# Optimization experiments

Measured on AMD Instinct MI355X. Metric: run time of the kernel, lower is better.

The kernel has to match this reference:

```python
import jax, jax.numpy as jnp
from jax import lax
import numpy as np

B, T, I, H, O = 2048, 512, 3, 128, 2


def _uniform(key, shape, scale):
    return jax.random.uniform(key, shape, jnp.float32, -scale, scale)


def setup_inputs() -> dict:
    key = jax.random.key(0)
    ks = jax.random.split(key, 12)
    s = 1.0 / np.sqrt(H)  # PyTorch LSTM init scale
    inp = {
        "x": jax.random.normal(ks[0], (B, T, I), jnp.float32),
        # layer 0: input size I
        "w_ih0": _uniform(ks[1], (4 * H, I), s),
        "w_hh0": _uniform(ks[2], (4 * H, H), s),
        "b_ih0": _uniform(ks[3], (4 * H,), s),
        "b_hh0": _uniform(ks[4], (4 * H,), s),
        # layer 1: input size H
        "w_ih1": _uniform(ks[5], (4 * H, H), s),
        "w_hh1": _uniform(ks[6], (4 * H, H), s),
        "b_ih1": _uniform(ks[7], (4 * H,), s),
        "b_hh1": _uniform(ks[8], (4 * H,), s),
        # final projection
        "fc_w": _uniform(ks[9], (O, H), 1.0 / np.sqrt(H)),
        "fc_b": _uniform(ks[10], (O,), 1.0 / np.sqrt(H)),
    }
    return inp


def _lstm_layer(x, w_ih, w_hh, b_ih, b_hh):
    # x: [B, T, D_in] -> hidden sequence [B, T, H]
    b, t, _ = x.shape
    h_dim = w_hh.shape[1]
    # precompute input projections for all timesteps (one big GEMM)
    x_proj = jnp.einsum("btd,gd->btg", x, w_ih) + b_ih + b_hh  # [B, T, 4H]
    x_proj = jnp.swapaxes(x_proj, 0, 1)  # [T, B, 4H]

    def step(carry, xt):
        h, c = carry
        gates = xt + h @ w_hh.T  # [B, 4H]
        i, f, g, o = jnp.split(gates, 4, axis=-1)  # PyTorch gate order i,f,g,o
        i = jax.nn.sigmoid(i)
        f = jax.nn.sigmoid(f)
        g = jnp.tanh(g)
        o = jax.nn.sigmoid(o)
        c = f * c + i * g
        h = o * jnp.tanh(c)
        return (h, c), h

    h0 = jnp.zeros((b, h_dim), x.dtype)
    c0 = jnp.zeros((b, h_dim), x.dtype)
    _, hs = lax.scan(step, (h0, c0), x_proj)  # hs: [T, B, H]
    return jnp.swapaxes(hs, 0, 1)  # [B, T, H]


def reference(x, w_ih0, w_hh0, b_ih0, b_hh0, w_ih1, w_hh1, b_ih1, b_hh1, fc_w, fc_b):
    h1 = _lstm_layer(x, w_ih0, w_hh0, b_ih0, b_hh0)   # [B, T, H]
    h2 = _lstm_layer(h1, w_ih1, w_hh1, b_ih1, b_hh1)  # [B, T, H]
    last = h2[:, -1, :]                                # [B, H]
    return last @ fc_w.T + fc_b                        # [B, O]
```

## Files before the change

### kernel.cpp

```cpp
#include <hip/hip_runtime.h>

#define B_   2048
#define T_   512
#define H_   128
#define G_   512
#define R_   8
#define NTHR 512

typedef _Float16 f16;
typedef _Float16 f16x8 __attribute__((ext_vector_type(8)));
typedef float    f32x4 __attribute__((ext_vector_type(4)));
typedef int      i32x2 __attribute__((ext_vector_type(2)));

#define OFF_W1    0
#define OFF_RING  131072
#define OFF_HB    139264
#define OFF_XT    143360
#define LDS_BYTES 145408

__device__ __forceinline__ float rcp_(float v) {
#if __has_builtin(__builtin_amdgcn_rcpf)
  return __builtin_amdgcn_rcpf(v);
#else
  return 1.0f / v;
#endif
}
__device__ __forceinline__ float sig_(float v)  { return rcp_(1.0f + __expf(-v)); }
__device__ __forceinline__ float tanh_(float v) { return 1.0f - 2.0f * rcp_(__expf(2.0f * v) + 1.0f); }

__device__ __forceinline__ f16x8 cvt8(const float* __restrict__ p) {
  float4 a = ((const float4*)p)[0];
  float4 b = ((const float4*)p)[1];
  f16x8 v;
  v[0]=(f16)a.x; v[1]=(f16)a.y; v[2]=(f16)a.z; v[3]=(f16)a.w;
  v[4]=(f16)b.x; v[5]=(f16)b.y; v[6]=(f16)b.z; v[7]=(f16)b.w;
  return v;
}
__device__ __forceinline__ f32x4 mfma16(f16x8 a, f16x8 b, f32x4 c) {
  return __builtin_amdgcn_mfma_f32_16x16x32_f16(a, b, c, 0, 0, 0);
}

__device__ __forceinline__ void pls2_(float a, float b, float& x, float& y) {
#if __has_builtin(__builtin_amdgcn_permlane32_swap)
  i32x2 r = __builtin_amdgcn_permlane32_swap(__float_as_int(a), __float_as_int(b),
                                             false, false);
  x = __int_as_float(r.x); y = __int_as_float(r.y);
#else
  asm volatile("v_permlane32_swap_b32 %0, %1" : "+v"(a), "+v"(b));
  x = a; y = b;
#endif
}

__global__ __launch_bounds__(NTHR, 2)
void lstm_v11(const float* __restrict__ x,
              const float* __restrict__ w_ih0, const float* __restrict__ w_hh0,
              const float* __restrict__ b_ih0, const float* __restrict__ b_hh0,
              const float* __restrict__ w_ih1, const float* __restrict__ w_hh1,
              const float* __restrict__ b_ih1, const float* __restrict__ b_hh1,
              const float* __restrict__ fc_w,  const float* __restrict__ fc_b,
              float* __restrict__ out)
{
  extern __shared__ char lds[];
  char*  w1L   = lds + OFF_W1;
  char*  ringB = lds + OFF_RING;
  char*  hBB   = lds + OFF_HB;
  char*  xT    = lds + OFF_XT;

  const int tid  = (int)threadIdx.x;
  const int lane = tid & 63;
  const int wv   = tid >> 6;
  const int n    = lane & 15;
  const int hi   = lane >> 4;
  const int u0   = wv * 16;
  const int blk  = (int)blockIdx.x;
  const int rsw  = (n & 7) << 4;

  for (int idx = tid; idx < 8192; idx += NTHR) {
    const int g  = idx >> 4, c  = idx & 15;
    const int w  = (g >> 4) & 7, nn = g & 15, q = g >> 7;
    const int kc = c >> 2,  hh = c & 3;
    f16x8 v = cvt8(w_ih1 + g*H_ + c*8);
    *(f16x8*)(w1L + w*16384 + (q*4+kc)*1024 + ((hh<<4) + nn)*16) = v;
  }
  for (int i = tid; i < 3584; i += NTHR) ((unsigned*)ringB)[i] = 0u;
  __syncthreads();

  float xr0 = 0.f, xr1 = 0.f, xr2 = 0.f;
  if (wv == 7) {
    const int tok = lane >> 3, r = lane & 7;
    const size_t base = (size_t)(blk*R_ + r) * T_;
    const float a0 = x[(base + tok)*3+0];
    const float a1 = x[(base + tok)*3+1];
    const float a2 = x[(base + tok)*3+2];
    f16* w = (f16*)(xT + tok*128 + r*16);
    w[0] = (f16)a0; w[1] = (f16)a1; w[2] = (f16)a2;
    xr0 = x[(base + 8 + tok)*3+0];
    xr1 = x[(base + 8 + tok)*3+1];
    xr2 = x[(base + 8 + tok)*3+2];
  }

  f16x8 whh0f[4][4], whh1f[4][4];
  #pragma unroll
  for (int q = 0; q < 4; ++q)
    #pragma unroll
    for (int kc = 0; kc < 4; ++kc) {
      const int off = (q*H_ + u0 + n)*H_ + kc*32 + hi*8;
      whh0f[q][kc] = cvt8(w_hh0 + off);
      whh1f[q][kc] = cvt8(w_hh1 + off);
    }
  f16x8 w0p[4];
  float b0[4], bP[4];
  #pragma unroll
  for (int q = 0; q < 4; ++q) {
    const int g = q*H_ + u0 + n;
    b0[q] = b_ih0[g] + b_hh0[g];
    bP[q] = b_ih1[g] + b_hh1[g];
    f16x8 z;
    #pragma unroll
    for (int e = 0; e < 8; ++e) z[e] = (f16)0.f;
    if (hi == 0) {
      z[0] = (f16)w_ih0[g*3+0];
      z[1] = (f16)w_ih0[g*3+1];
      z[2] = (f16)w_ih0[g*3+2];
    }
    w0p[q] = z;
  }

  int offA[4];
  #pragma unroll
  for (int kc = 0; kc < 4; ++kc)
    offA[kc] = (n&7)*256 + ((kc*64 + hi*16) ^ rsw);

  float cA0 = 0.f, cA1 = 0.f, cB0 = 0.f, cB1 = 0.f;
  f32x4 xpP[4];
  const int rowbase = (hi & 1)*4 + ((lane >= 32) ? 2 : 0);
  const int colb    = 2*(u0 + n);
  const int wOff0 = rowbase*256     + (colb ^ (rowbase<<4));
  const int wOff1 = (rowbase+1)*256 + (colb ^ ((rowbase+1)<<4));
  const char* __restrict__ w1lane = w1L + wv*16384 + lane*16;
  __syncthreads();

  auto xstage = [&](int s) {
    if (wv == 7 && (s & 7) == 3) {
      const int c = s >> 3;
      const int tok = lane >> 3, r = lane & 7;
      if (c <= 61) {
        const size_t base = (size_t)(blk*R_ + r) * T_ + (8*(c+2) + tok);
        const float a0 = x[base*3+0], a1 = x[base*3+1], a2 = x[base*3+2];
        f16* w = (f16*)(xT + ((c+1)&1)*1024 + tok*128 + r*16);
        w[0] = (f16)xr0; w[1] = (f16)xr1; w[2] = (f16)xr2;
        xr0 = a0; xr1 = a1; xr2 = a2;
      } else if (c == 62) {
        f16* w = (f16*)(xT + ((c+1)&1)*1024 + tok*128 + r*16);
        w[0] = (f16)xr0; w[1] = (f16)xr1; w[2] = (f16)xr2;
      }
    }
  };

  auto proj = [&](int s) {
    if ((s & 1) == 0 && s >= 2 && s <= T_) {
      const char* pa = ringB + ((n < 8) ? (((s-2)&3)*2048) : (((s-1)&3)*2048));
      #pragma unroll
      for (int q = 0; q < 4; ++q)
        { xpP[q][0]=bP[q]; xpP[q][1]=bP[q]; xpP[q][2]=bP[q]; xpP[q][3]=bP[q]; }
      #pragma unroll
      for (int kc = 0; kc < 4; ++kc) {
        const f16x8 a = *(const f16x8*)(pa + offA[kc]);
        #pragma unroll
        for (int q = 0; q < 4; ++q) {
          const f16x8 bf = *(const f16x8*)(w1lane + (q*4 + kc)*1024);
          xpP[q] = mfma16(a, bf, xpP[q]);
        }
      }
    }
  };

  auto l0 = [&](int s) {
    if (s < T_) {
      const f16x8 ax = *(const f16x8*)(xT + ((s>>3)&1)*1024 + (s&7)*128 + (n&7)*16);
      f32x4 acc[4];
      #pragma unroll
      for (int q = 0; q < 4; ++q) {
        f32x4 a; a[0]=b0[q]; a[1]=b0[q]; a[2]=b0[q]; a[3]=b0[q];
        acc[q] = mfma16(ax, w0p[q], a);
      }
      const char* pa = ringB + (((s-1)&3)*2048);
      #pragma unroll
      for (int kc = 0; kc < 4; ++kc) {
        const f16x8 af = *(const f16x8*)(pa + offA[kc]);
        #pragma unroll
        for (int q = 0; q < 4; ++q) acc[q] = mfma16(af, whh0f[q][kc], acc[q]);
      }
      char* wr = ringB + ((s&3)*2048);
      float gA[4], gB[4], d0, d1;
      #pragma unroll
      for (int q = 0; q < 4; ++q) {
        pls2_(acc[q][0], acc[q][2], gA[q], d0);
        pls2_(acc[q][1], acc[q][3], gB[q], d1);
      }
      {
        const float iv = sig_(gA[0]), fv = sig_(gA[1]), gv = tanh_(gA[2]), ov = sig_(gA[3]);
        cA0 = fv*cA0 + iv*gv;
        *(f16*)(wr + wOff0) = (f16)(ov * tanh_(cA0));
      }
      {
        const float iv = sig_(gB[0]), fv = sig_(gB[1]), gv = tanh_(gB[2]), ov = sig_(gB[3]);
        cA1 = fv*cA1 + iv*gv;
        *(f16*)(wr + wOff1) = (f16)(ov * tanh_(cA1));
      }
    }
  };

  auto l1 = [&](int s) {
    if (s >= 2) {
      const bool odd = (s & 1);
      const char* pb = hBB + (s&1)*2048;
      f32x4 acc[4];
      #pragma unroll
      for (int q = 0; q < 4; ++q) acc[q] = xpP[q];
      #pragma unroll
      for (int kc = 0; kc < 4; ++kc) {
        const f16x8 af = *(const f16x8*)(pb + offA[kc]);
        #pragma unroll
        for (int q = 0; q < 4; ++q) acc[q] = mfma16(af, whh1f[q][kc], acc[q]);
      }
      char* wr = hBB + (((s+1)&1)*2048);
      float gA[4], gB[4];
      #pragma unroll
      for (int q = 0; q < 4; ++q) {
        float ex, ey, fx, fy;
        pls2_(acc[q][0], acc[q][2], ex, ey);
        pls2_(acc[q][1], acc[q][3], fx, fy);
        gA[q] = odd ? ey : ex;
        gB[q] = odd ? fy : fx;
      }
      {
        const float iv = sig_(gA[0]), fv = sig_(gA[1]), gv = tanh_(gA[2]), ov = sig_(gA[3]);
        cB0 = fv*cB0 + iv*gv;
        *(f16*)(wr + wOff0) = (f16)(ov * tanh_(cB0));
      }
      {
        const float iv = sig_(gB[0]), fv = sig_(gB[1]), gv = tanh_(gB[2]), ov = sig_(gB[3]);
        cB1 = fv*cB1 + iv*gv;
        *(f16*)(wr + wOff1) = (f16)(ov * tanh_(cB1));
      }
    }
  };

  for (int s = 0; s < T_ + 2; ++s) {
    if (wv & 1) {
      xstage(s);
      l0(s);
      proj(s);
      l1(s);
    } else {
      proj(s);
      l1(s);
      l0(s);
    }
    __syncthreads();
  }

  if (tid < R_*2) {
    const int r = tid >> 1, o = tid & 1;
    float acc = fc_b[o];
    #pragma unroll 4
    for (int d = 0; d < H_; ++d) {
      const f16 hv = *(const f16*)(hBB + r*256 + ((2*d) ^ ((r&7)<<4)));
      acc += (float)hv * fc_w[o*H_ + d];
    }
    out[(blk*R_ + r)*2 + o] = acc;
  }
}

extern "C" void kernel_launch(void* const* d_in, const int* in_sizes, int n_in,
                              void* d_out, int out_size, void* d_ws, size_t ws_size,
                              hipStream_t stream) {
  const float* x     = (const float*)d_in[0];
  const float* w_ih0 = (const float*)d_in[1];
  const float* w_hh0 = (const float*)d_in[2];
  const float* b_ih0 = (const float*)d_in[3];
  const float* b_hh0 = (const float*)d_in[4];
  const float* w_ih1 = (const float*)d_in[5];
  const float* w_hh1 = (const float*)d_in[6];
  const float* b_ih1 = (const float*)d_in[7];
  const float* b_hh1 = (const float*)d_in[8];
  const float* fc_w  = (const float*)d_in[9];
  const float* fc_b  = (const float*)d_in[10];
  (void)in_sizes; (void)n_in; (void)out_size; (void)d_ws; (void)ws_size;

  hipFuncSetAttribute((const void*)lstm_v11,
                      hipFuncAttributeMaxDynamicSharedMemorySize, LDS_BYTES);

  lstm_v11<<<B_/R_, NTHR, LDS_BYTES, stream>>>(
      x, w_ih0, w_hh0, b_ih0, b_hh0, w_ih1, w_hh1, b_ih1, b_hh1,
      fc_w, fc_b, (float*)d_out);
}
```

Before: 857.2 us.

## Split layer-0 and layer-1 LSTM work across separate wave groups

The block grows to 1024 threads. Waves 0-7 run the layer-0 recurrence and waves 8-15 run the layer-1 input projection and recurrence, where before every wave interleaved both layers. The layer-0 input projection now uses a K=16 MFMA with the bias folded in as a constant-one input column, and the xT staging buffer doubles in size. The aim is to shorten each wave's serial per-step chain and halve per-wave register pressure. In exchange, each SIMD hosts more waves and every step synchronises 16 waves at the barrier.

```diff
diff --git a/kernel.cpp b/kernel.cpp
--- a/kernel.cpp
+++ b/kernel.cpp
@@ -5,9 +5,10 @@
 #define H_   128
 #define G_   512
 #define R_   8
-#define NTHR 512
+#define NTHR 1024
 
 typedef _Float16 f16;
+typedef _Float16 f16x4 __attribute__((ext_vector_type(4)));
 typedef _Float16 f16x8 __attribute__((ext_vector_type(8)));
 typedef float    f32x4 __attribute__((ext_vector_type(4)));
 typedef int      i32x2 __attribute__((ext_vector_type(2)));
@@ -16,7 +17,7 @@
 #define OFF_RING  131072
 #define OFF_HB    139264
 #define OFF_XT    143360
-#define LDS_BYTES 145408
+#define LDS_BYTES 147456
 
 __device__ __forceinline__ float rcp_(float v) {
 #if __has_builtin(__builtin_amdgcn_rcpf)
@@ -38,6 +39,9 @@
 }
 __device__ __forceinline__ f32x4 mfma16(f16x8 a, f16x8 b, f32x4 c) {
   return __builtin_amdgcn_mfma_f32_16x16x32_f16(a, b, c, 0, 0, 0);
+}
+__device__ __forceinline__ f32x4 mfma16k16(f16x4 a, f16x4 b, f32x4 c) {
+  return __builtin_amdgcn_mfma_f32_16x16x16f16(a, b, c, 0, 0, 0);
 }
 
 __device__ __forceinline__ void pls2_(float a, float b, float& x, float& y) {
@@ -51,8 +55,8 @@
 #endif
 }
 
-__global__ __launch_bounds__(NTHR, 2)
-void lstm_v11(const float* __restrict__ x,
+__global__ __launch_bounds__(NTHR)
+void lstm_v12(const float* __restrict__ x,
               const float* __restrict__ w_ih0, const float* __restrict__ w_hh0,
               const float* __restrict__ b_ih0, const float* __restrict__ b_hh0,
               const float* __restrict__ w_ih1, const float* __restrict__ w_hh1,
@@ -71,7 +75,7 @@
   const int wv   = tid >> 6;
   const int n    = lane & 15;
   const int hi   = lane >> 4;
-  const int u0   = wv * 16;
+  const int u0   = (wv & 7) * 16;
   const int blk  = (int)blockIdx.x;
   const int rsw  = (n & 7) << 4;
 
@@ -82,183 +86,175 @@
     f16x8 v = cvt8(w_ih1 + g*H_ + c*8);
     *(f16x8*)(w1L + w*16384 + (q*4+kc)*1024 + ((hh<<4) + nn)*16) = v;
   }
-  for (int i = tid; i < 3584; i += NTHR) ((unsigned*)ringB)[i] = 0u;
-  __syncthreads();
-
-  float xr0 = 0.f, xr1 = 0.f, xr2 = 0.f;
-  if (wv == 7) {
-    const int tok = lane >> 3, r = lane & 7;
-    const size_t base = (size_t)(blk*R_ + r) * T_;
-    const float a0 = x[(base + tok)*3+0];
-    const float a1 = x[(base + tok)*3+1];
-    const float a2 = x[(base + tok)*3+2];
-    f16* w = (f16*)(xT + tok*128 + r*16);
-    w[0] = (f16)a0; w[1] = (f16)a1; w[2] = (f16)a2;
-    xr0 = x[(base + 8 + tok)*3+0];
-    xr1 = x[(base + 8 + tok)*3+1];
-    xr2 = x[(base + 8 + tok)*3+2];
-  }
-
-  f16x8 whh0f[4][4], whh1f[4][4];
-  #pragma unroll
-  for (int q = 0; q < 4; ++q)
-    #pragma unroll
-    for (int kc = 0; kc < 4; ++kc) {
-      const int off = (q*H_ + u0 + n)*H_ + kc*32 + hi*8;
-      whh0f[q][kc] = cvt8(w_hh0 + off);
-      whh1f[q][kc] = cvt8(w_hh1 + off);
-    }
-  f16x8 w0p[4];
-  float b0[4], bP[4];
-  #pragma unroll
-  for (int q = 0; q < 4; ++q) {
-    const int g = q*H_ + u0 + n;
-    b0[q] = b_ih0[g] + b_hh0[g];
-    bP[q] = b_ih1[g] + b_hh1[g];
-    f16x8 z;
-    #pragma unroll
-    for (int e = 0; e < 8; ++e) z[e] = (f16)0.f;
-    if (hi == 0) {
-      z[0] = (f16)w_ih0[g*3+0];
-      z[1] = (f16)w_ih0[g*3+1];
-      z[2] = (f16)w_ih0[g*3+2];
-    }
-    w0p[q] = z;
-  }
+  for (int i = tid; i < 4096; i += NTHR) ((unsigned*)ringB)[i] = 0u;
 
   int offA[4];
   #pragma unroll
   for (int kc = 0; kc < 4; ++kc)
     offA[kc] = (n&7)*256 + ((kc*64 + hi*16) ^ rsw);
-
-  float cA0 = 0.f, cA1 = 0.f, cB0 = 0.f, cB1 = 0.f;
-  f32x4 xpP[4];
   const int rowbase = (hi & 1)*4 + ((lane >= 32) ? 2 : 0);
   const int colb    = 2*(u0 + n);
   const int wOff0 = rowbase*256     + (colb ^ (rowbase<<4));
   const int wOff1 = (rowbase+1)*256 + (colb ^ ((rowbase+1)<<4));
-  const char* __restrict__ w1lane = w1L + wv*16384 + lane*16;
   __syncthreads();
 
-  auto xstage = [&](int s) {
-    if (wv == 7 && (s & 7) == 3) {
-      const int c = s >> 3;
+  if (wv < 8) {
+    float xr0 = 0.f, xr1 = 0.f, xr2 = 0.f;
+    if (wv == 7) {
       const int tok = lane >> 3, r = lane & 7;
-      if (c <= 61) {
-        const size_t base = (size_t)(blk*R_ + r) * T_ + (8*(c+2) + tok);
-        const float a0 = x[base*3+0], a1 = x[base*3+1], a2 = x[base*3+2];
-        f16* w = (f16*)(xT + ((c+1)&1)*1024 + tok*128 + r*16);
-        w[0] = (f16)xr0; w[1] = (f16)xr1; w[2] = (f16)xr2;
-        xr0 = a0; xr1 = a1; xr2 = a2;
-      } else if (c == 62) {
-        f16* w = (f16*)(xT + ((c+1)&1)*1024 + tok*128 + r*16);
-        w[0] = (f16)xr0; w[1] = (f16)xr1; w[2] = (f16)xr2;
-      }
-    }
-  };
-
-  auto proj = [&](int s) {
-    if ((s & 1) == 0 && s >= 2 && s <= T_) {
-      const char* pa = ringB + ((n < 8) ? (((s-2)&3)*2048) : (((s-1)&3)*2048));
+      const size_t base = (size_t)(blk*R_ + r) * T_;
+      f16x4 v; v[0] = (f16)x[(base + tok)*3+0];
+               v[1] = (f16)x[(base + tok)*3+1];
+               v[2] = (f16)x[(base + tok)*3+2];
+               v[3] = (f16)1.f;
+      *(f16x4*)(xT + tok*256 + r*32) = v;
+      xr0 = x[(base + 8 + tok)*3+0];
+      xr1 = x[(base + 8 + tok)*3+1];
+      xr2 = x[(base + 8 + tok)*3+2];
+    }
+    f16x8 whh0f[4][4];
+    #pragma unroll
+    for (int q = 0; q < 4; ++q)
       #pragma unroll
-      for (int q = 0; q < 4; ++q)
-        { xpP[q][0]=bP[q]; xpP[q][1]=bP[q]; xpP[q][2]=bP[q]; xpP[q][3]=bP[q]; }
+      for (int kc = 0; kc < 4; ++kc)
+        whh0f[q][kc] = cvt8(w_hh0 + (q*H_ + u0 + n)*H_ + kc*32 + hi*8);
+    f16x4 w0px[4];
+    #pragma unroll
+    for (int q = 0; q < 4; ++q) {
+      const int g = q*H_ + u0 + n;
+      f16x4 z; z[0]=(f16)0.f; z[1]=(f16)0.f; z[2]=(f16)0.f; z[3]=(f16)0.f;
+      if (hi == 0) {
+        z[0] = (f16)w_ih0[g*3+0];
+        z[1] = (f16)w_ih0[g*3+1];
+        z[2] = (f16)w_ih0[g*3+2];
+        z[3] = (f16)(b_ih0[g] + b_hh0[g]);
+      }
+      w0px[q] = z;
+    }
+    float cA0 = 0.f, cA1 = 0.f;
+    __syncthreads();
+
+    for (int s = 0; s < T_ + 2; ++s) {
+      if (wv == 7 && (s & 7) == 3) {
+        const int c = s >> 3;
+        const int tok = lane >> 3, r = lane & 7;
+        if (c <= 61) {
+          const size_t base = (size_t)(blk*R_ + r) * T_ + (8*(c+2) + tok);
+          const float a0 = x[base*3+0], a1 = x[base*3+1], a2 = x[base*3+2];
+          f16x4 v; v[0]=(f16)xr0; v[1]=(f16)xr1; v[2]=(f16)xr2; v[3]=(f16)1.f;
+          *(f16x4*)(xT + ((c+1)&1)*2048 + tok*256 + r*32) = v;
+          xr0 = a0; xr1 = a1; xr2 = a2;
+        } else if (c == 62) {
+          f16x4 v; v[0]=(f16)xr0; v[1]=(f16)xr1; v[2]=(f16)xr2; v[3]=(f16)1.f;
+          *(f16x4*)(xT + ((c+1)&1)*2048 + tok*256 + r*32) = v;
+        }
+      }
+      if (s < T_) {
+        const f16x4 ax = *(const f16x4*)(xT + ((s>>3)&1)*2048 + (s&7)*256
+                                         + (n&7)*32 + hi*8);
+        f32x4 z4; z4[0]=0.f; z4[1]=0.f; z4[2]=0.f; z4[3]=0.f;
+        f32x4 acc[4];
+        #pragma unroll
+        for (int q = 0; q < 4; ++q) acc[q] = mfma16k16(ax, w0px[q], z4);
+        const char* pa = ringB + (((s-1)&3)*2048);
+        #pragma unroll
+        for (int kc = 0; kc < 4; ++kc) {
+          const f16x8 af = *(const f16x8*)(pa + offA[kc]);
+          #pragma unroll
+          for (int q = 0; q < 4; ++q) acc[q] = mfma16(af, whh0f[q][kc], acc[q]);
+        }
+        char* wr = ringB + ((s&3)*2048);
+        float gA[4], gB[4], d0, d1;
+        #pragma unroll
+        for (int q = 0; q < 4; ++q) {
+          pls2_(acc[q][0], acc[q][2], gA[q], d0);
+          pls2_(acc[q][1], acc[q][3], gB[q], d1);
+        }
+        {
+          const float iv = sig_(gA[0]), fv = sig_(gA[1]), gv = tanh_(gA[2]), ov = sig_(gA[3]);
+          cA0 = fv*cA0 + iv*gv;
+          *(f16*)(wr + wOff0) = (f16)(ov * tanh_(cA0));
+        }
+        {
+          const float iv = sig_(gB[0]), fv = sig_(gB[1]), gv = tanh_(gB[2]), ov = sig_(gB[3]);
+          cA1 = fv*cA1 + iv*gv;
+          *(f16*)(wr + wOff1) = (f16)(ov * tanh_(cA1));
+        }
+      }
+      __syncthreads();
+    }
+  } else {
+    f16x8 whh1f[4][4];
+    #pragma unroll
+    for (int q = 0; q < 4; ++q)
       #pragma unroll
-      for (int kc = 0; kc < 4; ++kc) {
-        const f16x8 a = *(const f16x8*)(pa + offA[kc]);
+      for (int kc = 0; kc < 4; ++kc)
+        whh1f[q][kc] = cvt8(w_hh1 + (q*H_ + u0 + n)*H_ + kc*32 + hi*8);
+    float bP[4];
+    #pragma unroll
+    for (int q = 0; q < 4; ++q) {
+      const int g = q*H_ + u0 + n;
+      bP[q] = b_ih1[g] + b_hh1[g];
+    }
+    float cB0 = 0.f, cB1 = 0.f;
+    f32x4 xpP[4];
+    const char* __restrict__ w1lane = w1L + (wv & 7)*16384 + lane*16;
+    __syncthreads();
+
+    for (int s = 0; s < T_ + 2; ++s) {
+      if ((s & 1) == 0 && s >= 2 && s <= T_) {
+        const char* pa = ringB + ((n < 8) ? (((s-2)&3)*2048) : (((s-1)&3)*2048));
+        #pragma unroll
+        for (int q = 0; q < 4; ++q)
+          { xpP[q][0]=bP[q]; xpP[q][1]=bP[q]; xpP[q][2]=bP[q]; xpP[q][3]=bP[q]; }
+        #pragma unroll
+        for (int kc = 0; kc < 4; ++kc) {
+          const f16x8 a = *(const f16x8*)(pa + offA[kc]);
+          #pragma unroll
+          for (int q = 0; q < 4; ++q) {
+            const f16x8 bf = *(const f16x8*)(w1lane + (q*4 + kc)*1024);
+            xpP[q] = mfma16(a, bf, xpP[q]);
+          }
+        }
+      }
+      if (s >= 2) {
+        const bool odd = (s & 1);
+        const char* pb = hBB + (s&1)*2048;
+        f32x4 acc[4];
+        {
+          const f16x8 af = *(const f16x8*)(pb + offA[0]);
+          #pragma unroll
+          for (int q = 0; q < 4; ++q) acc[q] = mfma16(af, whh1f[q][0], xpP[q]);
+        }
+        #pragma unroll
+        for (int kc = 1; kc < 4; ++kc) {
+          const f16x8 af = *(const f16x8*)(pb + offA[kc]);
+          #pragma unroll
+          for (int q = 0; q < 4; ++q) acc[q] = mfma16(af, whh1f[q][kc], acc[q]);
+        }
+        char* wr = hBB + (((s+1)&1)*2048);
+        float gA[4], gB[4];
         #pragma unroll
         for (int q = 0; q < 4; ++q) {
-          const f16x8 bf = *(const f16x8*)(w1lane + (q*4 + kc)*1024);
-          xpP[q] = mfma16(a, bf, xpP[q]);
-        }
-      }
-    }
-  };
-
-  auto l0 = [&](int s) {
-    if (s < T_) {
-      const f16x8 ax = *(const f16x8*)(xT + ((s>>3)&1)*1024 + (s&7)*128 + (n&7)*16);
-      f32x4 acc[4];
-      #pragma unroll
-      for (int q = 0; q < 4; ++q) {
-        f32x4 a; a[0]=b0[q]; a[1]=b0[q]; a[2]=b0[q]; a[3]=b0[q];
-        acc[q] = mfma16(ax, w0p[q], a);
-      }
-      const char* pa = ringB + (((s-1)&3)*2048);
-      #pragma unroll
-      for (int kc = 0; kc < 4; ++kc) {
-        const f16x8 af = *(const f16x8*)(pa + offA[kc]);
-        #pragma unroll
-        for (int q = 0; q < 4; ++q) acc[q] = mfma16(af, whh0f[q][kc], acc[q]);
-      }
-      char* wr = ringB + ((s&3)*2048);
-      float gA[4], gB[4], d0, d1;
-      #pragma unroll
-      for (int q = 0; q < 4; ++q) {
-        pls2_(acc[q][0], acc[q][2], gA[q], d0);
-        pls2_(acc[q][1], acc[q][3], gB[q], d1);
-      }
-      {
-        const float iv = sig_(gA[0]), fv = sig_(gA[1]), gv = tanh_(gA[2]), ov = sig_(gA[3]);
-        cA0 = fv*cA0 + iv*gv;
-        *(f16*)(wr + wOff0) = (f16)(ov * tanh_(cA0));
-      }
-      {
-        const float iv = sig_(gB[0]), fv = sig_(gB[1]), gv = tanh_(gB[2]), ov = sig_(gB[3]);
-        cA1 = fv*cA1 + iv*gv;
-        *(f16*)(wr + wOff1) = (f16)(ov * tanh_(cA1));
-      }
-    }
-  };
-
-  auto l1 = [&](int s) {
-    if (s >= 2) {
-      const bool odd = (s & 1);
-      const char* pb = hBB + (s&1)*2048;
-      f32x4 acc[4];
-      #pragma unroll
-      for (int q = 0; q < 4; ++q) acc[q] = xpP[q];
-      #pragma unroll
-      for (int kc = 0; kc < 4; ++kc) {
-        const f16x8 af = *(const f16x8*)(pb + offA[kc]);
-        #pragma unroll
-        for (int q = 0; q < 4; ++q) acc[q] = mfma16(af, whh1f[q][kc], acc[q]);
-      }
-      char* wr = hBB + (((s+1)&1)*2048);
-      float gA[4], gB[4];
-      #pragma unroll
-      for (int q = 0; q < 4; ++q) {
-        float ex, ey, fx, fy;
-        pls2_(acc[q][0], acc[q][2], ex, ey);
-        pls2_(acc[q][1], acc[q][3], fx, fy);
-        gA[q] = odd ? ey : ex;
-        gB[q] = odd ? fy : fx;
-      }
-      {
-        const float iv = sig_(gA[0]), fv = sig_(gA[1]), gv = tanh_(gA[2]), ov = sig_(gA[3]);
-        cB0 = fv*cB0 + iv*gv;
-        *(f16*)(wr + wOff0) = (f16)(ov * tanh_(cB0));
-      }
-      {
-        const float iv = sig_(gB[0]), fv = sig_(gB[1]), gv = tanh_(gB[2]), ov = sig_(gB[3]);
-        cB1 = fv*cB1 + iv*gv;
-        *(f16*)(wr + wOff1) = (f16)(ov * tanh_(cB1));
-      }
-    }
-  };
-
-  for (int s = 0; s < T_ + 2; ++s) {
-    if (wv & 1) {
-      xstage(s);
-      l0(s);
-      proj(s);
-      l1(s);
-    } else {
-      proj(s);
-      l1(s);
-      l0(s);
-    }
-    __syncthreads();
+          float ex, ey, fx, fy;
+          pls2_(acc[q][0], acc[q][2], ex, ey);
+          pls2_(acc[q][1], acc[q][3], fx, fy);
+          gA[q] = odd ? ey : ex;
+          gB[q] = odd ? fy : fx;
+        }
+        {
+          const float iv = sig_(gA[0]), fv = sig_(gA[1]), gv = tanh_(gA[2]), ov = sig_(gA[3]);
+          cB0 = fv*cB0 + iv*gv;
+          *(f16*)(wr + wOff0) = (f16)(ov * tanh_(cB0));
+        }
+        {
+          const float iv = sig_(gB[0]), fv = sig_(gB[1]), gv = tanh_(gB[2]), ov = sig_(gB[3]);
+          cB1 = fv*cB1 + iv*gv;
+          *(f16*)(wr + wOff1) = (f16)(ov * tanh_(cB1));
+        }
+      }
+      __syncthreads();
+    }
   }
 
   if (tid < R_*2) {
@@ -289,10 +285,10 @@
   const float* fc_b  = (const float*)d_in[10];
   (void)in_sizes; (void)n_in; (void)out_size; (void)d_ws; (void)ws_size;
 
-  hipFuncSetAttribute((const void*)lstm_v11,
+  hipFuncSetAttribute((const void*)lstm_v12,
                       hipFuncAttributeMaxDynamicSharedMemorySize, LDS_BYTES);
 
-  lstm_v11<<<B_/R_, NTHR, LDS_BYTES, stream>>>(
+  lstm_v12<<<B_/R_, NTHR, LDS_BYTES, stream>>>(
       x, w_ih0, w_hh0, b_ih0, b_hh0, w_ih1, w_hh1, b_ih1, b_hh1,
       fc_w, fc_b, (float*)d_out);
 }
```

Result: faster. 716.3 us (-16.4%).
